# Kernel tuning notes

Hardware: AMD Instinct MI355X
Metric: run time of the kernel (lower is better)

Reference implementation:

```python
import jax, jax.numpy as jnp
import numpy as np

EMBED_DIM = 1024
SCALE = 1.0 / float(np.sqrt(EMBED_DIM))


def setup_inputs() -> dict:
    key = jax.random.key(0)
    ks = jax.random.split(key, 7)
    B, S, D = 4, 2048, EMBED_DIM
    init = 1.0 / np.sqrt(D)
    x = jax.random.normal(ks[0], (B, S, D), dtype=jnp.float32)
    Wq = jax.random.uniform(ks[1], (D, D), jnp.float32, -init, init)
    bq = jax.random.uniform(ks[2], (D,), jnp.float32, -init, init)
    Wk = jax.random.uniform(ks[3], (D, D), jnp.float32, -init, init)
    bk = jax.random.uniform(ks[4], (D,), jnp.float32, -init, init)
    Wv = jax.random.uniform(ks[5], (D, D), jnp.float32, -init, init)
    bv = jax.random.uniform(ks[6], (D,), jnp.float32, -init, init)
    return {"x": x, "Wq": Wq, "bq": bq, "Wk": Wk, "bk": bk, "Wv": Wv, "bv": bv}


def reference(x, Wq, bq, Wk, bk, Wv, bv):
    # Linear projections (torch Linear: x @ W.T + b; here W stored as [in, out])
    q = x @ Wq + bq  # [B, S, D]
    k = x @ Wk + bk
    v = x @ Wv + bv
    # Manual scaled dot-product attention (single head)
    scores = jnp.einsum("bsd,btd->bst", q, k) * SCALE  # [B, S, S]
    attn = jax.nn.softmax(scores, axis=-1)
    # Dropout is identity at inference (eval mode); p=0.1 at train time.
    return jnp.einsum("bst,btd->bsd", attn, v)
```

## Files before the change

### kernel.cpp

```cpp
#include <hip/hip_runtime.h>

#define MODE_QKV 0
#define MODE_S   1
#define MODE_PV  2

typedef __attribute__((ext_vector_type(8))) short short8;
typedef __attribute__((ext_vector_type(4))) float floatx4;

typedef const unsigned __attribute__((address_space(1)))* gp_t;
typedef unsigned __attribute__((address_space(3)))* lp_t;

__device__ __forceinline__ void async16(const void* g, void* l) {
  __builtin_amdgcn_global_load_lds((gp_t)g, (lp_t)l, 16, 0, 0);
}

__device__ __forceinline__ void bar_raw() {
  asm volatile("s_barrier" ::: "memory");
}

__device__ __forceinline__ unsigned short f2bf(float f) {
  union { float f; unsigned u; } x; x.f = f;
  unsigned r = x.u + 0x7fffu + ((x.u >> 16) & 1u);
  return (unsigned short)(r >> 16);
}
__device__ __forceinline__ float bf2f(unsigned short h) {
  union { unsigned u; float f; } x; x.u = ((unsigned)h) << 16;
  return x.f;
}


__device__ __forceinline__ void stage_half(const unsigned short* gp, long rowbase,
                                           int ldk, int kb, char* region,
                                           int wave, int lane) {
  const int rs = lane >> 3;
  const int kc = ((lane & 7) ^ rs) << 3;
  #pragma unroll
  for (int h = 0; h < 2; h++) {
    const int rr = (h * 8 + wave) * 8 + rs;
    async16(gp + (rowbase + rr) * (long)ldk + kb + kc,
            region + (h * 8 + wave) * 1024);
  }
}

__device__ __forceinline__ short8 frag(const char* region, int hr, int ks, int quad) {
  return *(const short8*)(region + hr * 128 + ((((ks << 2) | quad) ^ (hr & 7)) << 4));
}

#define MFMA_QUAD(MH, NH)                                                    \
  do {                                                                       \
    _Pragma("unroll")                                                        \
    for (int mi_ = 0; mi_ < 4; mi_++) {                                      \
      _Pragma("unroll")                                                      \
      for (int jj_ = 0; jj_ < 2; jj_++) {                                    \
        _Pragma("unroll")                                                    \
        for (int ks_ = 0; ks_ < 2; ks_++) {                                  \
          acc[MH][mi_][NH][jj_] = __builtin_amdgcn_mfma_f32_16x16x32_bf16(   \
              a[mi_][ks_], b[NH][jj_][ks_], acc[MH][mi_][NH][jj_], 0, 0, 0); \
        }                                                                    \
      }                                                                      \
    }                                                                        \
  } while (0)

template<int MODE>
__global__ __launch_bounds__(512, 1)
void gemm256(const unsigned short* __restrict__ A,
             const unsigned short* __restrict__ Bmat,
             const float* __restrict__ b0, const float* __restrict__ b1,
             const float* __restrict__ b2,
             unsigned short* __restrict__ O0, unsigned short* __restrict__ O1,
             unsigned short* __restrict__ O2, float* __restrict__ Of,
             float* __restrict__ lsum,
             int M, int N, int K, long aZ, long bZ, long cZ, float scale)
{
  __shared__ __attribute__((aligned(128))) char lds[131072];

  const int tid = threadIdx.x;
  const int wave = tid >> 6, lane = tid & 63;
  const int wm = wave >> 2, wn = wave & 3;
  const int quad = lane >> 4, l16 = lane & 15;

  const int gx = gridDim.x, gy = gridDim.y;
  int z, bm, bn;
  {
    int f = (blockIdx.z * gy + blockIdx.y) * gx + blockIdx.x;
    int T = gx * gy * (int)gridDim.z;
    int nsq = T >> 7;
    int xcd = f & 7, i = f >> 3;
    int sq = xcd * nsq + (i >> 4);
    int w = i & 15;
    int spz = (gx >> 2) * (gy >> 2);
    z = sq / spz;
    int sqr = sq - z * spz;
    int sqm = sqr / (gx >> 2), sqn = sqr - sqm * (gx >> 2);
    bm = (sqm * 4 + (w >> 2)) * 256;
    bn = (sqn * 4 + (w & 3)) * 256;
  }

  const unsigned short* Ap = (MODE == MODE_QKV) ? A : (A + (long)z * aZ);
  const unsigned short* Bp = Bmat + (long)z * bZ;

  const int NT = K >> 6;

  stage_half(Ap, bm,       K, 0,  lds +     0, wave, lane);
  stage_half(Bp, bn,       K, 0,  lds + 32768, wave, lane);
  stage_half(Bp, bn + 128, K, 0,  lds + 49152, wave, lane);
  stage_half(Ap, bm + 128, K, 0,  lds + 16384, wave, lane);
  stage_half(Ap, bm,       K, 64, lds + 65536 +     0, wave, lane);
  stage_half(Bp, bn,       K, 64, lds + 65536 + 32768, wave, lane);
  stage_half(Bp, bn + 128, K, 64, lds + 65536 + 49152, wave, lane);
  asm volatile("s_waitcnt vmcnt(6)" ::: "memory");
  bar_raw();

  floatx4 acc[2][4][2][2];
  #pragma unroll
  for (int p = 0; p < 2; p++)
    #pragma unroll
    for (int q2 = 0; q2 < 4; q2++)
      #pragma unroll
      for (int r = 0; r < 2; r++)
        #pragma unroll
        for (int s = 0; s < 2; s++)
          acc[p][q2][r][s] = (floatx4){0.f, 0.f, 0.f, 0.f};

  short8 a[4][2];
  short8 b[2][2][2];

  for (int j = 0; j < NT; j++) {
    char* bufc = lds + ((j & 1) << 16);
    char* bufn = lds + (((j + 1) & 1) << 16);
    const bool lp = (j + 2 >= NT);
    const int kn  = (j + 1) << 6;
    const int kn2 = (j + 2) << 6;

    #pragma unroll
    for (int mi = 0; mi < 4; mi++)
      #pragma unroll
      for (int ks = 0; ks < 2; ks++)
        a[mi][ks] = frag(bufc, wm * 64 + mi * 16 + l16, ks, quad);
    #pragma unroll
    for (int jj = 0; jj < 2; jj++)
      #pragma unroll
      for (int ks = 0; ks < 2; ks++)
        b[0][jj][ks] = frag(bufc + 32768, wn * 32 + jj * 16 + l16, ks, quad);
    if (j + 1 < NT)
      stage_half(Ap, bm + 128, K, kn, bufn + 16384, wave, lane);
    bar_raw();
    asm volatile("s_waitcnt lgkmcnt(0)" ::: "memory");
    __builtin_amdgcn_s_setprio(1);
    MFMA_QUAD(0, 0);
    __builtin_amdgcn_s_setprio(0);
    bar_raw();

    #pragma unroll
    for (int jj = 0; jj < 2; jj++)
      #pragma unroll
      for (int ks = 0; ks < 2; ks++)
        b[1][jj][ks] = frag(bufc + 49152, wn * 32 + jj * 16 + l16, ks, quad);
    if (!lp)
      stage_half(Ap, bm, K, kn2, bufc, wave, lane);
    bar_raw();
    asm volatile("s_waitcnt lgkmcnt(0)" ::: "memory");
    __builtin_amdgcn_s_setprio(1);
    MFMA_QUAD(0, 1);
    __builtin_amdgcn_s_setprio(0);
    bar_raw();

    #pragma unroll
    for (int mi = 0; mi < 4; mi++)
      #pragma unroll
      for (int ks = 0; ks < 2; ks++)
        a[mi][ks] = frag(bufc + 16384, wm * 64 + mi * 16 + l16, ks, quad);
    if (!lp)
      stage_half(Bp, bn, K, kn2, bufc + 32768, wave, lane);
    bar_raw();
    asm volatile("s_waitcnt lgkmcnt(0)" ::: "memory");
    __builtin_amdgcn_s_setprio(1);
    MFMA_QUAD(1, 0);
    __builtin_amdgcn_s_setprio(0);
    bar_raw();

    if (!lp) {
      stage_half(Bp, bn + 128, K, kn2, bufc + 49152, wave, lane);
      asm volatile("s_waitcnt vmcnt(6)" ::: "memory");
    } else {
      asm volatile("s_waitcnt vmcnt(0)" ::: "memory");
    }
    bar_raw();
    __builtin_amdgcn_s_setprio(1);
    MFMA_QUAD(1, 1);
    __builtin_amdgcn_s_setprio(0);
    bar_raw();
  }

  if (MODE == MODE_PV) {
    #pragma unroll
    for (int mh = 0; mh < 2; mh++)
      #pragma unroll
      for (int mi = 0; mi < 4; mi++) {
        const int row0 = bm + mh * 128 + wm * 64 + mi * 16 + quad * 4;
        float inv[4];
        #pragma unroll
        for (int r = 0; r < 4; r++)
          inv[r] = 1.0f / lsum[(long)z * M + row0 + r];
        #pragma unroll
        for (int nh = 0; nh < 2; nh++)
          #pragma unroll
          for (int jj = 0; jj < 2; jj++) {
            const int col = bn + nh * 128 + wn * 32 + jj * 16 + l16;
            #pragma unroll
            for (int r = 0; r < 4; r++)
              Of[(long)z * cZ + (long)(row0 + r) * N + col] =
                  acc[mh][mi][nh][jj][r] * inv[r];
          }
      }
    return;
  }

  const bool vtrans = (MODE == MODE_QKV) && (z == 2);
  float bi[2][2];
  if (MODE == MODE_QKV) {
    const float* bias = (z == 0) ? b0 : ((z == 1) ? b1 : b2);
    #pragma unroll
    for (int nh = 0; nh < 2; nh++)
      #pragma unroll
      for (int jj = 0; jj < 2; jj++)
        bi[nh][jj] = bias[bn + nh * 128 + wn * 32 + jj * 16 + l16];
  }

  unsigned short* epi = (unsigned short*)lds;
  #pragma unroll
  for (int mh = 0; mh < 2; mh++) {
    #pragma unroll
    for (int mi = 0; mi < 4; mi++) {
      const int r0 = wm * 64 + mi * 16 + quad * 4;
      #pragma unroll
      for (int nh = 0; nh < 2; nh++)
        #pragma unroll
        for (int jj = 0; jj < 2; jj++) {
          const int col = nh * 128 + wn * 32 + jj * 16 + l16;
          if (MODE == MODE_S) {
            #pragma unroll
            for (int r = 0; r < 4; r++)
              epi[(r0 + r) * 264 + col] = f2bf(__expf(acc[mh][mi][nh][jj][r] * scale));
          } else if (!vtrans) {
            #pragma unroll
            for (int r = 0; r < 4; r++)
              epi[(r0 + r) * 264 + col] = f2bf(acc[mh][mi][nh][jj][r] + bi[nh][jj]);
          } else {
            #pragma unroll
            for (int r = 0; r < 4; r += 2) {
              unsigned lo = f2bf(acc[mh][mi][nh][jj][r] + bi[nh][jj]);
              unsigned hi = f2bf(acc[mh][mi][nh][jj][r + 1] + bi[nh][jj]);
              *(unsigned*)&epi[col * 136 + r0 + r] = lo | (hi << 16);
            }
          }
        }
    }
    __syncthreads();

    if (!vtrans) {
      #pragma unroll
      for (int it = 0; it < 8; it++) {
        int flat = it * 4096 + tid * 8;
        int rr = flat >> 8, cc = flat & 255;
        short8 vline = *(const short8*)&epi[rr * 264 + cc];
        long grow = bm + mh * 128 + rr;
        if (MODE == MODE_S) {
          union { short8 v; unsigned short u[8]; } t; t.v = vline;
          float s8 = 0.f;
          #pragma unroll
          for (int jq = 0; jq < 8; jq++) s8 += bf2f(t.u[jq]);
          s8 += __shfl_xor(s8, 1);
          s8 += __shfl_xor(s8, 2);
          s8 += __shfl_xor(s8, 4);
          s8 += __shfl_xor(s8, 8);
          s8 += __shfl_xor(s8, 16);
          if ((lane & 31) == 0) atomicAdd(&lsum[(long)z * M + grow], s8);
          *(short8*)&O0[(long)z * cZ + grow * N + bn + cc] = vline;
        } else {
          unsigned short* O = (z == 0) ? O0 : O1;
          *(short8*)&O[grow * N + bn + cc] = vline;
        }
      }
    } else {
      int bb = bm >> 11, s0 = bm & 2047;
      #pragma unroll
      for (int it = 0; it < 8; it++) {
        int flat = it * 4096 + tid * 8;
        int dd = flat >> 7, ss = flat & 127;
        short8 vline = *(const short8*)&epi[dd * 136 + ss];
        *(short8*)&O2[(long)bb * (1024L * 2048) + (long)(bn + dd) * 2048 + s0 + mh * 128 + ss] = vline;
      }
    }
    if (mh == 0) __syncthreads();
  }
}


union SmemU {
  struct { unsigned short A[2][4096]; unsigned short B[2][4096]; } st;
  unsigned short epi[128 * 136];
};

template<int MODE>
__global__ __launch_bounds__(256, 4)
void gemm_nt(const unsigned short* __restrict__ A,
             const unsigned short* __restrict__ Bmat,
             const float* __restrict__ b0, const float* __restrict__ b1,
             const float* __restrict__ b2,
             unsigned short* __restrict__ O0, unsigned short* __restrict__ O1,
             unsigned short* __restrict__ O2,
             float* __restrict__ Of, float* __restrict__ lsum,
             int M, int N, int K, long aZ, long bZ, long cZ, float scale)
{
  __shared__ SmemU smem;

  const int tid = threadIdx.x;
  const int wave = tid >> 6, lane = tid & 63;
  const int wm = wave >> 1, wn = wave & 1;
  const int quad = lane >> 4, l16 = lane & 15;

  const int gx = gridDim.x, gy = gridDim.y;
  int z, bm, bn;
  {
    int f = (blockIdx.z * gy + blockIdx.y) * gx + blockIdx.x;
    int T = gx * gy * (int)gridDim.z;
    int nsq = T >> 7;
    int xcd = f & 7, i = f >> 3;
    int sq = xcd * nsq + (i >> 4);
    int w = i & 15;
    int spz = (gx >> 2) * (gy >> 2);
    z = sq / spz;
    int sqr = sq - z * spz;
    int sqm = sqr / (gx >> 2), sqn = sqr - sqm * (gx >> 2);
    bm = (sqm * 4 + (w >> 2)) * 128;
    bn = (sqn * 4 + (w & 3)) * 128;
  }

  const unsigned short* Ap = (MODE == MODE_QKV) ? A : (A + (long)z * aZ);
  const unsigned short* Bp = Bmat + (long)z * bZ;

  floatx4 acc[4][4];
  #pragma unroll
  for (int i = 0; i < 4; i++)
    #pragma unroll
    for (int j = 0; j < 4; j++)
      acc[i][j] = (floatx4){0.f, 0.f, 0.f, 0.f};

  char* asb = (char*)&smem.st.A[0][0] + wave * 1024;
  char* bsb = (char*)&smem.st.B[0][0] + wave * 1024;

  for (int k0 = 0; k0 < K; k0 += 64) {
    #pragma unroll
    for (int p = 0; p < 2; p++) {
      #pragma unroll
      for (int h = 0; h < 2; h++) {
        int flat = tid + h * 256;
        int r = flat >> 2, c = (flat & 3) << 3;
        async16(Ap + (long)(bm + r) * K + k0 + p * 32 + c,
                asb + p * 8192 + h * 4096);
        async16(Bp + (long)(bn + r) * K + k0 + p * 32 + c,
                bsb + p * 8192 + h * 4096);
      }
    }
    __syncthreads();

    #pragma unroll
    for (int ks = 0; ks < 2; ks++) {
      short8 afr[4], bfr[4];
      #pragma unroll
      for (int i = 0; i < 4; i++)
        afr[i] = *(const short8*)&smem.st.A[ks][(wm * 64 + i * 16 + l16) * 32 + quad * 8];
      #pragma unroll
      for (int i = 0; i < 4; i++)
        bfr[i] = *(const short8*)&smem.st.B[ks][(wn * 64 + i * 16 + l16) * 32 + quad * 8];
      #pragma unroll
      for (int mi = 0; mi < 4; mi++)
        #pragma unroll
        for (int ni = 0; ni < 4; ni++)
          acc[mi][ni] = __builtin_amdgcn_mfma_f32_16x16x32_bf16(
              afr[mi], bfr[ni], acc[mi][ni], 0, 0, 0);
    }
    __syncthreads();
  }

  if (MODE == MODE_PV) {
    #pragma unroll
    for (int mi = 0; mi < 4; mi++) {
      int row0 = bm + wm * 64 + mi * 16 + quad * 4;
      float inv[4];
      #pragma unroll
      for (int r = 0; r < 4; r++)
        inv[r] = 1.0f / lsum[(long)z * M + row0 + r];
      #pragma unroll
      for (int ni = 0; ni < 4; ni++) {
        int col = bn + wn * 64 + ni * 16 + l16;
        #pragma unroll
        for (int r = 0; r < 4; r++)
          Of[(long)z * cZ + (long)(row0 + r) * N + col] = acc[mi][ni][r] * inv[r];
      }
    }
    return;
  }

  const bool vtrans = (MODE == MODE_QKV) && (z == 2);
  float bi[4];
  if (MODE == MODE_QKV) {
    const float* bias = (z == 0) ? b0 : ((z == 1) ? b1 : b2);
    #pragma unroll
    for (int ni = 0; ni < 4; ni++) bi[ni] = bias[bn + wn * 64 + ni * 16 + l16];
  }

  #pragma unroll
  for (int ni = 0; ni < 4; ni++) {
    int col = wn * 64 + ni * 16 + l16;
    float bb = (MODE == MODE_QKV) ? bi[ni] : 0.f;
    #pragma unroll
    for (int mi = 0; mi < 4; mi++) {
      int row0 = wm * 64 + mi * 16 + quad * 4;
      if (MODE == MODE_S) {
        #pragma unroll
        for (int r = 0; r < 4; r++)
          smem.epi[(row0 + r) * 136 + col] = f2bf(__expf(acc[mi][ni][r] * scale));
      } else if (!vtrans) {
        #pragma unroll
        for (int r = 0; r < 4; r++)
          smem.epi[(row0 + r) * 136 + col] = f2bf(acc[mi][ni][r] + bb);
      } else {
        #pragma unroll
        for (int r = 0; r < 4; r += 2) {
          unsigned lo = f2bf(acc[mi][ni][r] + bb);
          unsigned hi = f2bf(acc[mi][ni][r + 1] + bb);
          *(unsigned*)&smem.epi[col * 136 + row0 + r] = lo | (hi << 16);
        }
      }
    }
  }
  __syncthreads();

  #pragma unroll
  for (int i = 0; i < 8; i++) {
    int flat = i * 2048 + tid * 8;
    int rr = flat >> 7, cc = flat & 127;
    short8 vline = *(const short8*)&smem.epi[rr * 136 + cc];
    if (MODE == MODE_S) {
      union { short8 v; unsigned short u[8]; } t; t.v = vline;
      float s8 = 0.f;
      #pragma unroll
      for (int j = 0; j < 8; j++) s8 += bf2f(t.u[j]);
      s8 += __shfl_xor(s8, 1);
      s8 += __shfl_xor(s8, 2);
      s8 += __shfl_xor(s8, 4);
      s8 += __shfl_xor(s8, 8);
      if ((lane & 15) == 0) atomicAdd(&lsum[(long)z * M + bm + rr], s8);
      *(short8*)&O0[(long)z * cZ + (long)(bm + rr) * N + bn + cc] = vline;
    } else if (!vtrans) {
      unsigned short* O = (z == 0) ? O0 : O1;
      *(short8*)&O[(long)(bm + rr) * N + bn + cc] = vline;
    } else {
      int bb = bm >> 11, s0 = bm & 2047;
      *(short8*)&O2[(long)bb * (1024L * 2048) + (long)(bn + rr) * 2048 + s0 + cc] = vline;
    }
  }
}

__global__ __launch_bounds__(256)
void prep_kernel(const float* __restrict__ x, unsigned short* __restrict__ xb,
                 const float* __restrict__ W0, const float* __restrict__ W1,
                 const float* __restrict__ W2, unsigned short* __restrict__ Wt,
                 float* __restrict__ lsum) {
  int blk = blockIdx.x;
  if (blk < 4096) {
    long i = ((long)blk * 256 + threadIdx.x) * 8;
    float4 a = *(const float4*)(x + i);
    float4 b = *(const float4*)(x + i + 4);
    union { int4 v; unsigned short u[8]; } t;
    t.u[0] = f2bf(a.x); t.u[1] = f2bf(a.y); t.u[2] = f2bf(a.z); t.u[3] = f2bf(a.w);
    t.u[4] = f2bf(b.x); t.u[5] = f2bf(b.y); t.u[6] = f2bf(b.z); t.u[7] = f2bf(b.w);
    *(int4*)(xb + i) = t.v;
  } else if (blk < 7168) {
    __shared__ float tile[32][33];
    int tt = blk - 4096;
    int zz = tt >> 10, rem = tt & 1023;
    int kb = (rem >> 5) * 32, nb = (rem & 31) * 32;
    const float* W = (zz == 0) ? W0 : ((zz == 1) ? W1 : W2);
    unsigned short* O = Wt + (long)zz * 1024 * 1024;
    int t = threadIdx.x, tr = t >> 5, tc = t & 31;
    #pragma unroll
    for (int i = 0; i < 4; i++)
      tile[tr + i * 8][tc] = W[(long)(kb + tr + i * 8) * 1024 + nb + tc];
    __syncthreads();
    #pragma unroll
    for (int i = 0; i < 4; i++)
      O[(long)(nb + tr + i * 8) * 1024 + kb + tc] = f2bf(tile[tc][tr + i * 8]);
  } else {
    int i = (blk - 7168) * 256 + threadIdx.x;
    lsum[i] = 0.f;
  }
}

extern "C" void kernel_launch(void* const* d_in, const int* in_sizes, int n_in,
                              void* d_out, int out_size, void* d_ws, size_t ws_size,
                              hipStream_t stream) {
  const float* x  = (const float*)d_in[0];
  const float* Wq = (const float*)d_in[1];
  const float* bq = (const float*)d_in[2];
  const float* Wk = (const float*)d_in[3];
  const float* bk = (const float*)d_in[4];
  const float* Wv = (const float*)d_in[5];
  const float* bv = (const float*)d_in[6];
  float* out = (float*)d_out;

  const int B = 4, S = 2048, D = 1024;
  const int M = B * S;
  const float scale = 0.03125f;

  unsigned short* xb = (unsigned short*)d_out;
  unsigned short* Wt = xb + (size_t)M * D;
  unsigned short* q  = (unsigned short*)d_ws;
  unsigned short* k  = q + (size_t)M * D;
  unsigned short* vT = k + (size_t)M * D;
  unsigned short* P  = vT + (size_t)M * D;

  size_t need_full = ((size_t)3 * M * D + (size_t)B * S * S) * sizeof(unsigned short)
                   + (size_t)M * sizeof(float);
  const bool full = (ws_size >= need_full);
  float* lsum = full ? (float*)(P + (size_t)B * S * S)
                     : (float*)(P + (size_t)S * S);

  prep_kernel<<<7200, 256, 0, stream>>>(x, xb, Wq, Wk, Wv, Wt, lsum);

  gemm256<MODE_QKV><<<dim3(D / 256, M / 256, 3), 512, 0, stream>>>(
      xb, Wt, bq, bk, bv, q, k, vT, nullptr, nullptr,
      M, D, D, 0, (long)D * D, 0, 1.0f);

  if (full) {
    gemm256<MODE_S><<<dim3(S / 256, S / 256, B), 512, 0, stream>>>(
        q, k, nullptr, nullptr, nullptr, P, nullptr, nullptr, nullptr, lsum,
        S, S, D, (long)S * D, (long)S * D, (long)S * S, scale);
    gemm256<MODE_PV><<<dim3(D / 256, S / 256, B), 512, 0, stream>>>(
        P, vT, nullptr, nullptr, nullptr, nullptr, nullptr, nullptr, out, lsum,
        S, D, S, (long)S * S, (long)D * S, (long)S * D, 1.0f);
  } else {
    for (int b = 0; b < B; b++) {
      const unsigned short* qb = q + (size_t)b * S * D;
      const unsigned short* kb = k + (size_t)b * S * D;
      const unsigned short* vb = vT + (size_t)b * S * D;
      float* ob = out + (size_t)b * S * D;
      gemm_nt<MODE_S><<<dim3(S / 128, S / 128, 1), 256, 0, stream>>>(
          qb, kb, nullptr, nullptr, nullptr, P, nullptr, nullptr, nullptr,
          lsum + (size_t)b * S,
          S, S, D, 0, 0, 0, scale);
      gemm_nt<MODE_PV><<<dim3(D / 128, S / 128, 1), 256, 0, stream>>>(
          P, vb, nullptr, nullptr, nullptr, nullptr, nullptr, nullptr, ob,
          lsum + (size_t)b * S,
          S, D, S, 0, 0, 0, 1.0f);
    }
  }
}
```

Measured before the change: 257.9 us.

## Restructure 256-tile GEMM main loop into two phases with A-fragment double buffering

The main K-loop of the 256x256 GEMM kernel goes from four MFMA quadrants, each fenced by two barriers, to two phases that each cover a full 128-row half against both B halves. A fragments are double-buffered in registers (aX/aY), and the next tile's first A half is prefetched from LDS during the current iteration. Waits use partial lgkmcnt/vmcnt counts so LDS reads overlap the barrier. This cuts barriers per iteration from eight to two and lengthens uninterrupted MFMA runs. In exchange, register pressure rises from the extra fragment buffers, and the hand-tuned wait counts must match the number of outstanding loads exactly.

```diff
diff --git a/kernel.cpp b/kernel.cpp
--- a/kernel.cpp
+++ b/kernel.cpp
@@ -12,10 +12,6 @@
 
 __device__ __forceinline__ void async16(const void* g, void* l) {
   __builtin_amdgcn_global_load_lds((gp_t)g, (lp_t)l, 16, 0, 0);
-}
-
-__device__ __forceinline__ void bar_raw() {
-  asm volatile("s_barrier" ::: "memory");
 }
 
 __device__ __forceinline__ unsigned short f2bf(float f) {
@@ -46,16 +42,20 @@
   return *(const short8*)(region + hr * 128 + ((((ks << 2) | quad) ^ (hr & 7)) << 4));
 }
 
-#define MFMA_QUAD(MH, NH)                                                    \
+#define MFMA_PH(MH, AREG)                                                    \
   do {                                                                       \
     _Pragma("unroll")                                                        \
-    for (int mi_ = 0; mi_ < 4; mi_++) {                                      \
+    for (int ks_ = 0; ks_ < 2; ks_++) {                                      \
       _Pragma("unroll")                                                      \
-      for (int jj_ = 0; jj_ < 2; jj_++) {                                    \
+      for (int mi_ = 0; mi_ < 4; mi_++) {                                    \
         _Pragma("unroll")                                                    \
-        for (int ks_ = 0; ks_ < 2; ks_++) {                                  \
-          acc[MH][mi_][NH][jj_] = __builtin_amdgcn_mfma_f32_16x16x32_bf16(   \
-              a[mi_][ks_], b[NH][jj_][ks_], acc[MH][mi_][NH][jj_], 0, 0, 0); \
+        for (int nh_ = 0; nh_ < 2; nh_++) {                                  \
+          _Pragma("unroll")                                                  \
+          for (int jj_ = 0; jj_ < 2; jj_++) {                                \
+            acc[MH][mi_][nh_][jj_] = __builtin_amdgcn_mfma_f32_16x16x32_bf16(\
+                AREG[mi_][ks_], bb[nh_][jj_][ks_], acc[MH][mi_][nh_][jj_],   \
+                0, 0, 0);                                                    \
+          }                                                                  \
         }                                                                    \
       }                                                                      \
     }                                                                        \
@@ -109,7 +109,7 @@
   stage_half(Bp, bn,       K, 64, lds + 65536 + 32768, wave, lane);
   stage_half(Bp, bn + 128, K, 64, lds + 65536 + 49152, wave, lane);
   asm volatile("s_waitcnt vmcnt(6)" ::: "memory");
-  bar_raw();
+  asm volatile("s_barrier" ::: "memory");
 
   floatx4 acc[2][4][2][2];
   #pragma unroll
@@ -122,75 +122,70 @@
         for (int s = 0; s < 2; s++)
           acc[p][q2][r][s] = (floatx4){0.f, 0.f, 0.f, 0.f};
 
-  short8 a[4][2];
-  short8 b[2][2][2];
+  short8 aX[4][2];
+  short8 aY[4][2];
+  short8 bb[2][2][2];
+
+  #pragma unroll
+  for (int mi = 0; mi < 4; mi++)
+    #pragma unroll
+    for (int ks = 0; ks < 2; ks++)
+      aX[mi][ks] = frag(lds, wm * 64 + mi * 16 + l16, ks, quad);
 
   for (int j = 0; j < NT; j++) {
     char* bufc = lds + ((j & 1) << 16);
     char* bufn = lds + (((j + 1) & 1) << 16);
-    const bool lp = (j + 2 >= NT);
     const int kn  = (j + 1) << 6;
     const int kn2 = (j + 2) << 6;
 
     #pragma unroll
+    for (int nh = 0; nh < 2; nh++)
+      #pragma unroll
+      for (int jj = 0; jj < 2; jj++)
+        #pragma unroll
+        for (int ks = 0; ks < 2; ks++)
+          bb[nh][jj][ks] = frag(bufc + 32768 + nh * 16384,
+                                wn * 32 + jj * 16 + l16, ks, quad);
+    #pragma unroll
     for (int mi = 0; mi < 4; mi++)
       #pragma unroll
       for (int ks = 0; ks < 2; ks++)
-        a[mi][ks] = frag(bufc, wm * 64 + mi * 16 + l16, ks, quad);
-    #pragma unroll
-    for (int jj = 0; jj < 2; jj++)
-      #pragma unroll
-      for (int ks = 0; ks < 2; ks++)
-        b[0][jj][ks] = frag(bufc + 32768, wn * 32 + jj * 16 + l16, ks, quad);
+        aY[mi][ks] = frag(bufc + 16384, wm * 64 + mi * 16 + l16, ks, quad);
+    asm volatile("s_waitcnt lgkmcnt(8)" ::: "memory");
+    asm volatile("s_barrier" ::: "memory");
     if (j + 1 < NT)
-      stage_half(Ap, bm + 128, K, kn, bufn + 16384, wave, lane);
-    bar_raw();
-    asm volatile("s_waitcnt lgkmcnt(0)" ::: "memory");
+      stage_half(Ap, bm + 128, K, kn,  bufn + 16384, wave, lane);
+    if (j + 2 < NT)
+      stage_half(Ap, bm,       K, kn2, bufc,         wave, lane);
     __builtin_amdgcn_s_setprio(1);
-    MFMA_QUAD(0, 0);
+    MFMA_PH(0, aX);
     __builtin_amdgcn_s_setprio(0);
-    bar_raw();
-
-    #pragma unroll
-    for (int jj = 0; jj < 2; jj++)
-      #pragma unroll
-      for (int ks = 0; ks < 2; ks++)
-        b[1][jj][ks] = frag(bufc + 49152, wn * 32 + jj * 16 + l16, ks, quad);
-    if (!lp)
-      stage_half(Ap, bm, K, kn2, bufc, wave, lane);
-    bar_raw();
-    asm volatile("s_waitcnt lgkmcnt(0)" ::: "memory");
-    __builtin_amdgcn_s_setprio(1);
-    MFMA_QUAD(0, 1);
-    __builtin_amdgcn_s_setprio(0);
-    bar_raw();
-
-    #pragma unroll
-    for (int mi = 0; mi < 4; mi++)
-      #pragma unroll
-      for (int ks = 0; ks < 2; ks++)
-        a[mi][ks] = frag(bufc + 16384, wm * 64 + mi * 16 + l16, ks, quad);
-    if (!lp)
-      stage_half(Bp, bn, K, kn2, bufc + 32768, wave, lane);
-    bar_raw();
-    asm volatile("s_waitcnt lgkmcnt(0)" ::: "memory");
-    __builtin_amdgcn_s_setprio(1);
-    MFMA_QUAD(1, 0);
-    __builtin_amdgcn_s_setprio(0);
-    bar_raw();
-
-    if (!lp) {
-      stage_half(Bp, bn + 128, K, kn2, bufc + 49152, wave, lane);
-      asm volatile("s_waitcnt vmcnt(6)" ::: "memory");
+
+    if (j + 2 < NT) {
+      asm volatile("s_waitcnt vmcnt(2)" ::: "memory");
     } else {
       asm volatile("s_waitcnt vmcnt(0)" ::: "memory");
     }
-    bar_raw();
+    if (j + 1 < NT) {
+      #pragma unroll
+      for (int mi = 0; mi < 4; mi++)
+        #pragma unroll
+        for (int ks = 0; ks < 2; ks++)
+          aX[mi][ks] = frag(bufn, wm * 64 + mi * 16 + l16, ks, quad);
+      asm volatile("s_waitcnt lgkmcnt(8)" ::: "memory");
+    } else {
+      asm volatile("s_waitcnt lgkmcnt(0)" ::: "memory");
+    }
+    asm volatile("s_barrier" ::: "memory");
+    if (j + 2 < NT) {
+      stage_half(Bp, bn,       K, kn2, bufc + 32768, wave, lane);
+      stage_half(Bp, bn + 128, K, kn2, bufc + 49152, wave, lane);
+    }
     __builtin_amdgcn_s_setprio(1);
-    MFMA_QUAD(1, 1);
+    MFMA_PH(1, aY);
     __builtin_amdgcn_s_setprio(0);
-    bar_raw();
-  }
+  }
+  __syncthreads();
 
   if (MODE == MODE_PV) {
     #pragma unroll
@@ -283,13 +278,13 @@
         }
       }
     } else {
-      int bb = bm >> 11, s0 = bm & 2047;
+      int bb2 = bm >> 11, s0 = bm & 2047;
       #pragma unroll
       for (int it = 0; it < 8; it++) {
         int flat = it * 4096 + tid * 8;
         int dd = flat >> 7, ss = flat & 127;
         short8 vline = *(const short8*)&epi[dd * 136 + ss];
-        *(short8*)&O2[(long)bb * (1024L * 2048) + (long)(bn + dd) * 2048 + s0 + mh * 128 + ss] = vline;
+        *(short8*)&O2[(long)bb2 * (1024L * 2048) + (long)(bn + dd) * 2048 + s0 + mh * 128 + ss] = vline;
       }
     }
     if (mh == 0) __syncthreads();
@@ -414,7 +409,7 @@
   #pragma unroll
   for (int ni = 0; ni < 4; ni++) {
     int col = wn * 64 + ni * 16 + l16;
-    float bb = (MODE == MODE_QKV) ? bi[ni] : 0.f;
+    float bbias = (MODE == MODE_QKV) ? bi[ni] : 0.f;
     #pragma unroll
     for (int mi = 0; mi < 4; mi++) {
       int row0 = wm * 64 + mi * 16 + quad * 4;
@@ -425,12 +420,12 @@
       } else if (!vtrans) {
         #pragma unroll
         for (int r = 0; r < 4; r++)
-          smem.epi[(row0 + r) * 136 + col] = f2bf(acc[mi][ni][r] + bb);
+          smem.epi[(row0 + r) * 136 + col] = f2bf(acc[mi][ni][r] + bbias);
       } else {
         #pragma unroll
         for (int r = 0; r < 4; r += 2) {
-          unsigned lo = f2bf(acc[mi][ni][r] + bb);
-          unsigned hi = f2bf(acc[mi][ni][r + 1] + bb);
+          unsigned lo = f2bf(acc[mi][ni][r] + bbias);
+          unsigned hi = f2bf(acc[mi][ni][r + 1] + bbias);
           *(unsigned*)&smem.epi[col * 136 + row0 + r] = lo | (hi << 16);
         }
       }
```

New measurement: 295.3 us. 14.5% more time.
